# Kernel optimization log

Measured on AMD Instinct MI355X. Metric: run time of the kernel, lower is better.

The kernel has to match this reference:

```python
import jax, jax.numpy as jnp
import numpy as np

N = 2097152
H = 64

def snake(x, a):
    # Snake activation: x + sin^2(a*x)/a, per-channel learnable a
    s = jnp.sin(a * x)
    return x + s * s / a

def _branch_params(key):
    ks = jax.random.split(key, 4)
    def lin(k, fan_in, fan_out):
        bound = 1.0 / np.sqrt(fan_in)
        kw, kb = jax.random.split(k)
        W = jax.random.uniform(kw, (fan_out, fan_in), jnp.float32, -bound, bound)
        b = jax.random.uniform(kb, (fan_out,), jnp.float32, -bound, bound)
        return W, b
    W1, b1 = lin(ks[0], 1, H)
    W2, b2 = lin(ks[1], H, H)
    W3, b3 = lin(ks[2], H, H)
    W4, b4 = lin(ks[3], H, 1)
    a1 = jnp.ones((H,), jnp.float32)
    a2 = jnp.ones((H,), jnp.float32)
    a3 = jnp.ones((H,), jnp.float32)
    return W1, b1, a1, W2, b2, a2, W3, b3, a3, W4, b4

def setup_inputs() -> dict:
    key = jax.random.key(0)
    kx, k1, k2 = jax.random.split(key, 3)
    x = jax.random.normal(kx, (N, 1), jnp.float32)
    p1 = _branch_params(k1)
    p2 = _branch_params(k2)
    names = ["W1", "b1", "a1", "W2", "b2", "a2", "W3", "b3", "a3", "W4", "b4"]
    d = {"x": x}
    for n, v in zip(names, p1):
        d[n + "_m1"] = v
    for n, v in zip(names, p2):
        d[n + "_m2"] = v
    return d

def _mlp(x, W1, b1, a1, W2, b2, a2, W3, b3, a3, W4, b4):
    h = snake(x @ W1.T + b1, a1)
    h = snake(h @ W2.T + b2, a2)
    h = snake(h @ W3.T + b3, a3)
    return h @ W4.T + b4

def reference(x,
              W1_m1, b1_m1, a1_m1, W2_m1, b2_m1, a2_m1, W3_m1, b3_m1, a3_m1, W4_m1, b4_m1,
              W1_m2, b1_m2, a1_m2, W2_m2, b2_m2, a2_m2, W3_m2, b3_m2, a3_m2, W4_m2, b4_m2):
    out1 = _mlp(x, W1_m1, b1_m1, a1_m1, W2_m1, b2_m1, a2_m1, W3_m1, b3_m1, a3_m1, W4_m1, b4_m1)
    out2 = _mlp(2.0 * x, W1_m2, b1_m2, a1_m2, W2_m2, b2_m2, a2_m2, W3_m2, b3_m2, a3_m2, W4_m2, b4_m2)
    return out1 + out2
```

## Files before the change

kernel.cpp:

```cpp
#include <hip/hip_runtime.h>


typedef __fp16 h8v __attribute__((ext_vector_type(8)));
typedef __fp16 h2v __attribute__((ext_vector_type(2)));
typedef __attribute__((ext_vector_type(4))) float f4v;

union H8U { h8v v; h2v p[4]; };

#define MFMA16(a, b, c) __builtin_amdgcn_mfma_f32_16x16x32_f16((a), (b), (c), 0, 0, 0)

__device__ __forceinline__ void act_frags(f4v (&acc)[4], h8v (&B)[2]) {
    #pragma unroll
    for (int t = 0; t < 4; ++t) {
        #pragma unroll
        for (int j = 0; j < 4; ++j) {
            float q = acc[t][j];
            float s = __sinf(q);
            acc[t][j] = fmaf(s, s, q);
        }
    }
    #pragma unroll
    for (int s2 = 0; s2 < 2; ++s2) {
        H8U u;
        u.p[0] = __builtin_amdgcn_cvt_pkrtz(acc[2 * s2][0],     acc[2 * s2][1]);
        u.p[1] = __builtin_amdgcn_cvt_pkrtz(acc[2 * s2][2],     acc[2 * s2][3]);
        u.p[2] = __builtin_amdgcn_cvt_pkrtz(acc[2 * s2 + 1][0], acc[2 * s2 + 1][1]);
        u.p[3] = __builtin_amdgcn_cvt_pkrtz(acc[2 * s2 + 1][2], acc[2 * s2 + 1][3]);
        B[s2] = u.v;
    }
}

__global__ __launch_bounds__(256, 2) void mlp_fused(
    const float* __restrict__ x,
    const float* __restrict__ W1a, const float* __restrict__ b1a, const float* __restrict__ a1a,
    const float* __restrict__ W2a, const float* __restrict__ b2a, const float* __restrict__ a2a,
    const float* __restrict__ W3a, const float* __restrict__ b3a, const float* __restrict__ a3a,
    const float* __restrict__ W4a, const float* __restrict__ b4a,
    const float* __restrict__ W1b, const float* __restrict__ b1b, const float* __restrict__ a1b,
    const float* __restrict__ W2b, const float* __restrict__ b2b, const float* __restrict__ a2b,
    const float* __restrict__ W3b, const float* __restrict__ b3b, const float* __restrict__ a3b,
    const float* __restrict__ W4b, const float* __restrict__ b4b,
    float* __restrict__ out, int n)
{
    const int lane = threadIdx.x & 63;
    const int col  = lane & 15;
    const int g    = lane >> 4;
    const int br   = (int)(blockIdx.x & 1);
    const int sub  = (int)(blockIdx.x >> 1);
    const int wid  = sub * 4 + (int)(threadIdx.x >> 6);
    const int nwaves = (int)((gridDim.x >> 1) << 2);
    const int nst = n >> 5;
    const float xscale = br ? 2.0f : 1.0f;

    const float* W1 = br ? W1b : W1a;  const float* b1 = br ? b1b : b1a;  const float* a1 = br ? a1b : a1a;
    const float* W2 = br ? W2b : W2a;  const float* b2 = br ? b2b : b2a;  const float* a2 = br ? a2b : a2a;
    const float* W3 = br ? W3b : W3a;  const float* b3 = br ? b3b : b3a;  const float* a3 = br ? a3b : a3a;
    const float* W4 = br ? W4b : W4a;  const float* b4 = br ? b4b : b4a;

    f4v w1p[4], b1p[4];
    #pragma unroll
    for (int t = 0; t < 4; ++t) {
        const int c0 = 16 * t + 4 * g;
        const f4v a1v = *(const f4v*)(a1 + c0);
        w1p[t] = (a1v * xscale) * *(const f4v*)(W1 + c0);
        b1p[t] = a1v * *(const f4v*)(b1 + c0);
    }

    h8v W2f[4][2], W3f[4][2];
    #pragma unroll
    for (int L = 0; L < 2; ++L) {
        const float* W    = L ? W3 : W2;
        const float* aout = L ? a3 : a2;
        const float* ain  = L ? a2 : a1;
        #pragma unroll
        for (int s = 0; s < 2; ++s) {
            const int kb = 32 * s + 4 * g;
            const f4v aia = *(const f4v*)(ain + kb);
            const f4v aib = *(const f4v*)(ain + kb + 16);
            float ra[8];
            #pragma unroll
            for (int j = 0; j < 4; ++j) { ra[j] = 1.0f / aia[j]; ra[4 + j] = 1.0f / aib[j]; }
            #pragma unroll
            for (int t = 0; t < 4; ++t) {
                const int o = 16 * t + col;
                const f4v wa = *(const f4v*)(W + o * 64 + kb);
                const f4v wb = *(const f4v*)(W + o * 64 + kb + 16);
                const float ao = aout[o];
                h8v hh;
                #pragma unroll
                for (int j = 0; j < 8; ++j) {
                    const float wv = (j < 4) ? wa[j & 3] : wb[j & 3];
                    hh[j] = (__fp16)(ao * wv * ra[j]);
                }
                if (L == 0) W2f[t][s] = hh;
                else        W3f[t][s] = hh;
            }
        }
    }

    f4v bias2[4], bias3[4], w4p[4];
    #pragma unroll
    for (int t = 0; t < 4; ++t) {
        const int c0 = 16 * t + 4 * g;
        bias2[t] = *(const f4v*)(b2 + c0) * *(const f4v*)(a2 + c0);
        bias3[t] = *(const f4v*)(b3 + c0) * *(const f4v*)(a3 + c0);
        w4p[t]   = *(const f4v*)(W4 + c0) / *(const f4v*)(a3 + c0);
    }
    const float b4v = b4[0];

    int st = wid;
    if (st >= nst) return;
    float xA = x[st * 32 + col];
    float xB = x[st * 32 + 16 + col];

    while (st < nst) {
        const int snext = st + nwaves;
        float xAn = 0.0f, xBn = 0.0f;
        if (snext < nst) {
            xAn = x[snext * 32 + col];
            xBn = x[snext * 32 + 16 + col];
        }

        f4v accA[4], accB[4];
        #pragma unroll
        for (int t = 0; t < 4; ++t) {
            #pragma unroll
            for (int j = 0; j < 4; ++j) {
                accA[t][j] = fmaf(w1p[t][j], xA, b1p[t][j]);
                accB[t][j] = fmaf(w1p[t][j], xB, b1p[t][j]);
            }
        }
        h8v BA[2], BB[2];
        act_frags(accA, BA);
        act_frags(accB, BB);

        f4v acc2A[4], acc2B[4];
        #pragma unroll
        for (int t = 0; t < 4; ++t) {
            f4v dA = bias2[t], dB = bias2[t];
            #pragma unroll
            for (int s = 0; s < 2; ++s) {
                dA = MFMA16(W2f[t][s], BA[s], dA);
                dB = MFMA16(W2f[t][s], BB[s], dB);
            }
            acc2A[t] = dA; acc2B[t] = dB;
        }
        act_frags(acc2A, BA);
        act_frags(acc2B, BB);

        #pragma unroll
        for (int t = 0; t < 4; ++t) {
            f4v dA = bias3[t], dB = bias3[t];
            #pragma unroll
            for (int s = 0; s < 2; ++s) {
                dA = MFMA16(W3f[t][s], BA[s], dA);
                dB = MFMA16(W3f[t][s], BB[s], dB);
            }
            accA[t] = dA; accB[t] = dB;
        }
        #pragma unroll
        for (int t = 0; t < 4; ++t) {
            #pragma unroll
            for (int j = 0; j < 4; ++j) {
                float qA = accA[t][j], qB = accB[t][j];
                float sA = __sinf(qA), sB = __sinf(qB);
                accA[t][j] = fmaf(sA, sA, qA);
                accB[t][j] = fmaf(sB, sB, qB);
            }
        }

        float pA = 0.0f, pB = 0.0f;
        #pragma unroll
        for (int t = 0; t < 4; ++t) {
            #pragma unroll
            for (int j = 0; j < 4; ++j) {
                pA = fmaf(w4p[t][j], accA[t][j], pA);
                pB = fmaf(w4p[t][j], accB[t][j], pB);
            }
        }
        pA += __shfl_xor(pA, 16); pA += __shfl_xor(pA, 32);
        pB += __shfl_xor(pB, 16); pB += __shfl_xor(pB, 32);

        const float pW = (lane < 16) ? pA : pB;
        if (lane < 32) unsafeAtomicAdd(&out[st * 32 + (lane & 31)], pW + b4v);

        st = snext; xA = xAn; xB = xBn;
    }
}

extern "C" void kernel_launch(void* const* d_in, const int* in_sizes, int n_in,
                              void* d_out, int out_size, void* d_ws, size_t ws_size,
                              hipStream_t stream) {
    const float* x   = (const float*)d_in[0];
    const float* W1a = (const float*)d_in[1];
    const float* b1a = (const float*)d_in[2];
    const float* a1a = (const float*)d_in[3];
    const float* W2a = (const float*)d_in[4];
    const float* b2a = (const float*)d_in[5];
    const float* a2a = (const float*)d_in[6];
    const float* W3a = (const float*)d_in[7];
    const float* b3a = (const float*)d_in[8];
    const float* a3a = (const float*)d_in[9];
    const float* W4a = (const float*)d_in[10];
    const float* b4a = (const float*)d_in[11];
    const float* W1b = (const float*)d_in[12];
    const float* b1b = (const float*)d_in[13];
    const float* a1b = (const float*)d_in[14];
    const float* W2b = (const float*)d_in[15];
    const float* b2b = (const float*)d_in[16];
    const float* a2b = (const float*)d_in[17];
    const float* W3b = (const float*)d_in[18];
    const float* b3b = (const float*)d_in[19];
    const float* a3b = (const float*)d_in[20];
    const float* W4b = (const float*)d_in[21];
    const float* b4b = (const float*)d_in[22];

    const int n = in_sizes[0];
    float* out = (float*)d_out;

    (void)hipMemsetAsync(out, 0, (size_t)n * sizeof(float), stream);
    mlp_fused<<<1024, 256, 0, stream>>>(x,
                                        W1a, b1a, a1a, W2a, b2a, a2a,
                                        W3a, b3a, a3a, W4a, b4a,
                                        W1b, b1b, a1b, W2b, b2b, a2b,
                                        W3b, b3b, a3b, W4b, b4b,
                                        out, n);
}
```

Baseline: 164.2 us.

## Carry activations in revolution units and call raw v_sin_f32 directly

Rescales every pre-activation by 1/(2π), folding the factor into the layer-1 weights, the biases and the final W4 weights. This lets the kernel call the hardware v_sin_f32 instruction, which takes its input in revolutions, through inline asm instead of __sinf, dropping the per-element multiply by 1/(2π). It also reuses the layer-1 accumulator arrays for layer 2 and raises the launch-bounds occupancy hint from 2 to 3 blocks per CU, which tightens the per-thread register budget and risks spills. The snake term now needs an extra multiply (s*s*R2PI), and fp16 rounding of the scaled activations shifts precision slightly.

```diff
diff --git a/kernel.cpp b/kernel.cpp
--- a/kernel.cpp
+++ b/kernel.cpp
@@ -7,6 +7,15 @@
 
 union H8U { h8v v; h2v p[4]; };
 
+#define R2PI  0.15915494309189535f
+#define TWOPI 6.283185307179586f
+
+__device__ __forceinline__ float sin_rev(float x) {
+    float r;
+    asm("v_sin_f32 %0, %1" : "=v"(r) : "v"(x));
+    return r;
+}
+
 #define MFMA16(a, b, c) __builtin_amdgcn_mfma_f32_16x16x32_f16((a), (b), (c), 0, 0, 0)
 
 __device__ __forceinline__ void act_frags(f4v (&acc)[4], h8v (&B)[2]) {
@@ -15,8 +24,8 @@
         #pragma unroll
         for (int j = 0; j < 4; ++j) {
             float q = acc[t][j];
-            float s = __sinf(q);
-            acc[t][j] = fmaf(s, s, q);
+            float s = sin_rev(q);
+            acc[t][j] = fmaf(s * s, R2PI, q);
         }
     }
     #pragma unroll
@@ -30,7 +39,7 @@
     }
 }
 
-__global__ __launch_bounds__(256, 2) void mlp_fused(
+__global__ __launch_bounds__(256, 3) void mlp_fused(
     const float* __restrict__ x,
     const float* __restrict__ W1a, const float* __restrict__ b1a, const float* __restrict__ a1a,
     const float* __restrict__ W2a, const float* __restrict__ b2a, const float* __restrict__ a2a,
@@ -62,8 +71,8 @@
     for (int t = 0; t < 4; ++t) {
         const int c0 = 16 * t + 4 * g;
         const f4v a1v = *(const f4v*)(a1 + c0);
-        w1p[t] = (a1v * xscale) * *(const f4v*)(W1 + c0);
-        b1p[t] = a1v * *(const f4v*)(b1 + c0);
+        w1p[t] = (a1v * (xscale * R2PI)) * *(const f4v*)(W1 + c0);
+        b1p[t] = (a1v * R2PI) * *(const f4v*)(b1 + c0);
     }
 
     h8v W2f[4][2], W3f[4][2];
@@ -102,9 +111,9 @@
     #pragma unroll
     for (int t = 0; t < 4; ++t) {
         const int c0 = 16 * t + 4 * g;
-        bias2[t] = *(const f4v*)(b2 + c0) * *(const f4v*)(a2 + c0);
-        bias3[t] = *(const f4v*)(b3 + c0) * *(const f4v*)(a3 + c0);
-        w4p[t]   = *(const f4v*)(W4 + c0) / *(const f4v*)(a3 + c0);
+        bias2[t] = *(const f4v*)(b2 + c0) * *(const f4v*)(a2 + c0) * R2PI;
+        bias3[t] = *(const f4v*)(b3 + c0) * *(const f4v*)(a3 + c0) * R2PI;
+        w4p[t]   = *(const f4v*)(W4 + c0) / *(const f4v*)(a3 + c0) * TWOPI;
     }
     const float b4v = b4[0];
 
@@ -134,7 +143,6 @@
         act_frags(accA, BA);
         act_frags(accB, BB);
 
-        f4v acc2A[4], acc2B[4];
         #pragma unroll
         for (int t = 0; t < 4; ++t) {
             f4v dA = bias2[t], dB = bias2[t];
@@ -143,10 +151,10 @@
                 dA = MFMA16(W2f[t][s], BA[s], dA);
                 dB = MFMA16(W2f[t][s], BB[s], dB);
             }
-            acc2A[t] = dA; acc2B[t] = dB;
-        }
-        act_frags(acc2A, BA);
-        act_frags(acc2B, BB);
+            accA[t] = dA; accB[t] = dB;
+        }
+        act_frags(accA, BA);
+        act_frags(accB, BB);
 
         #pragma unroll
         for (int t = 0; t < 4; ++t) {
@@ -163,9 +171,9 @@
             #pragma unroll
             for (int j = 0; j < 4; ++j) {
                 float qA = accA[t][j], qB = accB[t][j];
-                float sA = __sinf(qA), sB = __sinf(qB);
-                accA[t][j] = fmaf(sA, sA, qA);
-                accB[t][j] = fmaf(sB, sB, qB);
+                float sA = sin_rev(qA), sB = sin_rev(qB);
+                accA[t][j] = fmaf(sA * sA, R2PI, qA);
+                accB[t][j] = fmaf(sB * sB, R2PI, qB);
             }
         }
 
```

New measurement: 231.3 us. 1.41x slower.
